# Kernel optimization log

Measured on AMD Instinct MI355X. Metric: run time of the kernel, lower is better.

## Reference

```python
import jax, jax.numpy as jnp
import numpy as np

NUM_HEADS = 16
HEAD_DIM = 64
MAX_REL = 128
NEG_INF = -1e30


def setup_inputs() -> dict:
    key = jax.random.key(0)
    ks = jax.random.split(key, 5)
    B, L, D = 2, 2048, 1024
    x = jax.random.normal(ks[0], (B, L, D), dtype=jnp.float32)
    key_padding_mask = jnp.zeros((B, L), dtype=bool)  # True = padded
    Wqkv = jax.random.normal(ks[1], (D, 3 * D), dtype=jnp.float32) * (D ** -0.5)
    bqkv = jnp.zeros((3 * D,), dtype=jnp.float32)
    Wout = jax.random.normal(ks[2], (D, D), dtype=jnp.float32) * (D ** -0.5)
    bout = jnp.zeros((D,), dtype=jnp.float32)
    bias_table = jax.random.normal(ks[3], (2 * MAX_REL + 1, NUM_HEADS), dtype=jnp.float32) * 0.02
    return {"x": x, "key_padding_mask": key_padding_mask, "Wqkv": Wqkv,
            "bqkv": bqkv, "Wout": Wout, "bout": bout, "bias_table": bias_table}


def _rel_bias(bias_table, L):
    # relative position index: clamp(k - q, -MAX_REL, MAX_REL) + MAX_REL -> [L, L]
    rel = jnp.arange(L)[None, :] - jnp.arange(L)[:, None]
    idx = jnp.clip(rel, -MAX_REL, MAX_REL) + MAX_REL
    return bias_table[idx].transpose(2, 0, 1)  # [H, L, L]


def reference(x, key_padding_mask, Wqkv, bqkv, Wout, bout, bias_table):
    B, L, D = x.shape
    H, hd = NUM_HEADS, HEAD_DIM
    qkv = x @ Wqkv + bqkv                      # [B, L, 3D]
    q, k, v = jnp.split(qkv, 3, axis=-1)
    q = q.reshape(B, L, H, hd).transpose(0, 2, 1, 3)  # [B, H, L, hd]
    k = k.reshape(B, L, H, hd).transpose(0, 2, 1, 3)
    v = v.reshape(B, L, H, hd).transpose(0, 2, 1, 3)
    scores = jnp.einsum('bhqd,bhkd->bhqk', q, k) * (hd ** -0.5)
    scores = scores + _rel_bias(bias_table, L)[None]   # [B, H, L, L]
    scores = jnp.where(key_padding_mask[:, None, None, :], NEG_INF, scores)
    attn = jax.nn.softmax(scores, axis=-1)
    out = jnp.einsum('bhqk,bhkd->bhqd', attn, v)       # [B, H, L, hd]
    out = out.transpose(0, 2, 1, 3).reshape(B, L, D)
    return out @ Wout + bout
```

## Files before the change

### kernel.cpp

```cpp
#include <hip/hip_runtime.h>
#include <hip/hip_bf16.h>
#include <stdint.h>

#define LSEQ 2048
#define BATCH 2
#define DMODEL 1024
#define NH 16
#define HD 64

typedef __attribute__((ext_vector_type(8))) short bf16x8;
typedef __attribute__((ext_vector_type(4))) float f32x4;

__device__ __forceinline__ short f2bf(float f) {
  union { float f; uint32_t u; } v; v.f = f;
  uint32_t r = v.u + 0x8000u;
  return (short)(r >> 16);
}

__device__ __forceinline__ uint32_t pack_bf16(float lo, float hi) {
  union { float f; uint32_t u; } a, b; a.f = lo; b.f = hi;
  uint32_t al = (a.u + 0x8000u) >> 16;
  uint32_t bh = (b.u + 0x8000u) & 0xFFFF0000u;
  return al | bh;
}

__device__ __forceinline__ float exp2_fast(float x) {
#if __has_builtin(__builtin_amdgcn_exp2f)
  return __builtin_amdgcn_exp2f(x);
#else
  float r; asm("v_exp_f32 %0, %1" : "=v"(r) : "v"(x)); return r;
#endif
}

__device__ __forceinline__ void gll16(const void* g, void* l) {
  __builtin_amdgcn_global_load_lds(
      (const __attribute__((address_space(1))) void*)g,
      (__attribute__((address_space(3))) void*)l, 16, 0, 0);
}

__global__ void cvt_bf16(const float* __restrict__ in, short* __restrict__ out, int n) {
  int i = (blockIdx.x * blockDim.x + threadIdx.x) * 4;
  if (i < n) {
    float4 v = *(const float4*)(in + i);
    short4 o;
    o.x = f2bf(v.x); o.y = f2bf(v.y); o.z = f2bf(v.z); o.w = f2bf(v.w);
    *(short4*)(out + i) = o;
  }
}

__global__ void transpose_cvt(const float* __restrict__ in, short* __restrict__ out,
                              int K, int N) {
  __shared__ float tile[32][33];
  int kb = blockIdx.x * 32, nb = blockIdx.y * 32;
  int tx = threadIdx.x & 31, ty = threadIdx.x >> 5;
  #pragma unroll
  for (int i = ty; i < 32; i += 8)
    tile[i][tx] = in[(size_t)(kb + i) * N + nb + tx];
  __syncthreads();
  #pragma unroll
  for (int i = ty; i < 32; i += 8)
    out[(size_t)(nb + i) * K + kb + tx] = f2bf(tile[tx][i]);
}

template <int EPI>
__global__ __launch_bounds__(256, 2) void gemm_bt(
    const short* __restrict__ A, const short* __restrict__ Bt,
    const float* __restrict__ bias, float* __restrict__ outf,
    short* __restrict__ q_out, short* __restrict__ k_out, short* __restrict__ v_out) {
  constexpr int K = 1024, BK = 32;
  __shared__ short Als[128 * BK];
  __shared__ short Bls[128 * BK];
  const int tid = threadIdx.x;
  const int lane = tid & 63;
  const int m0 = blockIdx.x * 128;
  const int n0 = blockIdx.y * 128;
  const int wid = tid >> 6;
  const int wm = (wid >> 1) * 64, wn = (wid & 1) * 64;

  f32x4 acc[4][4] = {};

  for (int kt = 0; kt < K / BK; ++kt) {
    const int k0 = kt * BK;
    __syncthreads();
    #pragma unroll
    for (int inst = 0; inst < 2; ++inst) {
      int c = inst * 256 + tid;
      int row = c >> 2, cc = (c & 3) * 8;
      gll16(A + (size_t)(m0 + row) * K + k0 + cc, Als + c * 8);
      gll16(Bt + (size_t)(n0 + row) * K + k0 + cc, Bls + c * 8);
    }
    __syncthreads();
    bf16x8 af[4], bfv[4];
    #pragma unroll
    for (int m = 0; m < 4; ++m)
      af[m] = *(const bf16x8*)(Als + (wm + m * 16 + (lane & 15)) * BK + (lane >> 4) * 8);
    #pragma unroll
    for (int n = 0; n < 4; ++n)
      bfv[n] = *(const bf16x8*)(Bls + (wn + n * 16 + (lane & 15)) * BK + (lane >> 4) * 8);
    #pragma unroll
    for (int m = 0; m < 4; ++m)
      #pragma unroll
      for (int n = 0; n < 4; ++n)
        acc[m][n] = __builtin_amdgcn_mfma_f32_16x16x32_bf16(af[m], bfv[n], acc[m][n], 0, 0, 0);
  }

  #pragma unroll
  for (int m = 0; m < 4; ++m) {
    #pragma unroll
    for (int n = 0; n < 4; ++n) {
      #pragma unroll
      for (int r = 0; r < 4; ++r) {
        int row = m0 + wm + m * 16 + (lane >> 4) * 4 + r;
        int col = n0 + wn + n * 16 + (lane & 15);
        float val = acc[m][n][r] + bias[col];
        if (EPI == 1) {
          outf[(size_t)row * DMODEL + col] = val;
        } else {
          int b = row >> 11, l = row & 2047;
          int which = col >> 10, rem = col & 1023;
          int hn = rem >> 6, d = rem & 63;
          size_t bh = (size_t)b * NH + hn;
          if (which == 0)       q_out[(bh * LSEQ + l) * HD + d] = f2bf(val * 0.1803368801f);
          else if (which == 1)  k_out[(bh * LSEQ + l) * HD + d] = f2bf(val);
          else                  v_out[(bh * HD + d) * LSEQ + l] = f2bf(val);
        }
      }
    }
  }
}

__global__ __launch_bounds__(256, 3) void attn_kernel(
    const short* __restrict__ qb, const short* __restrict__ kb,
    const short* __restrict__ vtb, const unsigned char* __restrict__ kpm,
    const float* __restrict__ bias_table, short* __restrict__ ob) {
  constexpr int NT = LSEQ / 64;
  __shared__ short Kls[2][64 * 64];
  __shared__ short Vls[2][64 * 64];
  __shared__ short Pls[4][16 * 64];
  __shared__ float biasc[257];
  __shared__ float maskls[LSEQ];
  __shared__ int flags[NT];

  const int tid = threadIdx.x, lane = tid & 63, wid = tid >> 6;
  const int g = lane >> 4, c = lane & 15;
  const int q0 = blockIdx.x * 64, h = blockIdx.y, b = blockIdx.z;
  const size_t bh = (size_t)b * NH + h;
  const short* qbase = qb + bh * LSEQ * HD;
  const short* kbase = kb + bh * LSEQ * HD;
  const short* vbase = vtb + bh * HD * LSEQ;

  const int qrow_frag = q0 + wid * 16 + c;
  bf16x8 qf[2];
  #pragma unroll
  for (int ks = 0; ks < 2; ++ks)
    qf[ks] = *(const bf16x8*)(qbase + (size_t)qrow_frag * HD + ks * 32 + g * 8);

  if (tid < NT) flags[tid] = 0;
  __syncthreads();
  for (int i = tid; i < 257; i += 256) biasc[i] = bias_table[i * NH + h] * 1.44269504f;
  for (int i = tid; i < LSEQ; i += 256) {
    unsigned char m = kpm[(size_t)b * LSEQ + i];
    maskls[i] = m ? -1e30f : 0.f;
    if (m) flags[i >> 6] = 1;
  }
  __syncthreads();
  const float cb_lo = biasc[0], cb_hi = biasc[256];
  int myflag = (lane < 32) ? flags[lane] : 0;
  const unsigned mbits = (unsigned)__ballot(myflag != 0);

  auto stage = [&](int t, int bbuf) {
    const int kv0s = t * 64;
    #pragma unroll
    for (int inst = 0; inst < 2; ++inst) {
      int cc0 = inst * 256 + tid;
      int row = cc0 >> 3, cc = cc0 & 7;
      int scc = cc ^ (row & 7);
      gll16(kbase + (size_t)(kv0s + row) * HD + scc * 8, &Kls[bbuf][cc0 * 8]);
      gll16(vbase + (size_t)row * LSEQ + kv0s + scc * 8, &Vls[bbuf][cc0 * 8]);
    }
  };

  f32x4 o[4], l_acc;
  #pragma unroll
  for (int nt = 0; nt < 4; ++nt) o[nt] = (f32x4){0.f, 0.f, 0.f, 0.f};
  l_acc = (f32x4){0.f, 0.f, 0.f, 0.f};

  bf16x8 onesf;
  #pragma unroll
  for (int j = 0; j < 8; ++j) onesf[j] = (short)0x3F80;

  char* pw = (char*)&Pls[wid][0];
  const int c7s = (c & 7) << 4;

  stage(0, 0);

  for (int t = 0; t < NT; ++t) {
    const int bb = t & 1;
    const int kv0 = t * 64;
    if (t < NT - 1) {
      stage(t + 1, bb ^ 1);
      asm volatile("s_waitcnt vmcnt(4) lgkmcnt(0)" ::: "memory");
    } else {
      asm volatile("s_waitcnt vmcnt(0) lgkmcnt(0)" ::: "memory");
    }
    __builtin_amdgcn_s_barrier();
    __builtin_amdgcn_sched_barrier(0);

    f32x4 st[4];
    #pragma unroll
    for (int nt = 0; nt < 4; ++nt) {
      f32x4 a = {};
      #pragma unroll
      for (int ks = 0; ks < 2; ++ks) {
        int krow = nt * 16 + c;
        int kbyte = (ks * 32 + g * 8) * 2;
        const bf16x8 kf =
            *(const bf16x8*)((const char*)&Kls[bb][0] + krow * 128 + (kbyte ^ ((krow & 7) << 4)));
        a = __builtin_amdgcn_mfma_f32_16x16x32_bf16(kf, qf[ks], a, 0, 0, 0);
      }
      st[nt] = a;
    }

    const int dqk = kv0 - q0;
    if (dqk >= 192 || dqk <= -192) {
      const float cb = dqk > 0 ? cb_hi : cb_lo;
      #pragma unroll
      for (int nt = 0; nt < 4; ++nt)
        #pragma unroll
        for (int r = 0; r < 4; ++r) st[nt][r] += cb;
    } else {
      const int q = q0 + wid * 16 + c;
      #pragma unroll
      for (int nt = 0; nt < 4; ++nt)
        #pragma unroll
        for (int r = 0; r < 4; ++r) {
          int rel = kv0 + nt * 16 + g * 4 + r - q;
          rel = rel < -128 ? -128 : (rel > 128 ? 128 : rel);
          st[nt][r] += biasc[rel + 128];
        }
    }
    if (mbits & (1u << t)) {
      #pragma unroll
      for (int nt = 0; nt < 4; ++nt)
        #pragma unroll
        for (int r = 0; r < 4; ++r)
          st[nt][r] += maskls[kv0 + nt * 16 + g * 4 + r];
    }

    #pragma unroll
    for (int nt = 0; nt < 4; ++nt) {
      uint32_t p01 = pack_bf16(exp2_fast(st[nt][0]), exp2_fast(st[nt][1]));
      uint32_t p23 = pack_bf16(exp2_fast(st[nt][2]), exp2_fast(st[nt][3]));
      uint2 w; w.x = p01; w.y = p23;
      *(uint2*)(pw + c * 128 + ((nt * 32 + g * 8) ^ c7s)) = w;
    }

    asm volatile("s_waitcnt lgkmcnt(0)" ::: "memory");
    __builtin_amdgcn_sched_barrier(0);

    #pragma unroll
    for (int ks = 0; ks < 2; ++ks) {
      const bf16x8 pa = *(const bf16x8*)(pw + c * 128 + ((ks * 64 + g * 16) ^ c7s));
      l_acc = __builtin_amdgcn_mfma_f32_16x16x32_bf16(pa, onesf, l_acc, 0, 0, 0);
      int pbyte = (ks * 32 + g * 8) * 2;
      #pragma unroll
      for (int nt = 0; nt < 4; ++nt) {
        int vrow = nt * 16 + c;
        const bf16x8 vf =
            *(const bf16x8*)((const char*)&Vls[bb][0] + vrow * 128 + (pbyte ^ ((vrow & 7) << 4)));
        o[nt] = __builtin_amdgcn_mfma_f32_16x16x32_bf16(pa, vf, o[nt], 0, 0, 0);
      }
    }

    __builtin_amdgcn_sched_barrier(0);
    __builtin_amdgcn_s_barrier();
  }

  #pragma unroll
  for (int r = 0; r < 4; ++r) {
    float inv = 1.f / l_acc[r];
    int qrow = q0 + wid * 16 + g * 4 + r;
    size_t obase = ((size_t)b * LSEQ + qrow) * DMODEL + (size_t)h * HD;
    #pragma unroll
    for (int nt = 0; nt < 4; ++nt)
      ob[obase + nt * 16 + c] = f2bf(o[nt][r] * inv);
  }
}

extern "C" void kernel_launch(void* const* d_in, const int* in_sizes, int n_in,
                              void* d_out, int out_size, void* d_ws, size_t ws_size,
                              hipStream_t stream) {
  (void)in_sizes; (void)n_in; (void)out_size; (void)ws_size;
  const float* x = (const float*)d_in[0];
  const unsigned char* kpm = (const unsigned char*)d_in[1];
  const float* Wqkv = (const float*)d_in[2];
  const float* bqkv = (const float*)d_in[3];
  const float* Wout = (const float*)d_in[4];
  const float* bout = (const float*)d_in[5];
  const float* btab = (const float*)d_in[6];
  float* out = (float*)d_out;

  short* ws = (short*)d_ws;
  short* xbf   = ws;
  short* wqkvT = xbf + 4194304;
  short* woutT = wqkvT + 3145728;
  short* qbuf  = woutT + 1048576;
  short* kbuf  = qbuf + 4194304;
  short* vtbuf = kbuf + 4194304;
  short* obuf  = vtbuf + 4194304;

  cvt_bf16<<<dim3(4096), dim3(256), 0, stream>>>(x, xbf, 4194304);
  transpose_cvt<<<dim3(32, 96), dim3(256), 0, stream>>>(Wqkv, wqkvT, 1024, 3072);
  transpose_cvt<<<dim3(32, 32), dim3(256), 0, stream>>>(Wout, woutT, 1024, 1024);

  gemm_bt<0><<<dim3(32, 24), dim3(256), 0, stream>>>(xbf, wqkvT, bqkv, nullptr,
                                                     qbuf, kbuf, vtbuf);
  attn_kernel<<<dim3(32, 16, 2), dim3(256), 0, stream>>>(qbuf, kbuf, vtbuf, kpm, btab, obuf);
  gemm_bt<1><<<dim3(32, 8), dim3(256), 0, stream>>>(obuf, woutT, bout, out,
                                                    nullptr, nullptr, nullptr);
}
```

Measured before the change: 156.5 us.

## Process 32 query rows per wave to reuse K/V tiles across two query groups

The attention kernel doubles its query tile from 64 to 128 rows per block. Each wave now handles two 16-row query groups, and every K and V fragment read from LDS feeds two MFMAs, halving K/V global and LDS traffic per query. The mask preprocessing is also simplified: a per-tile bitmask is built from vectorized byte loads, and the mask is read straight from global memory only on masked tiles, instead of a float mask array kept in LDS. In exchange the grid is half the size, register pressure is higher, and launch bounds drop to 2 blocks per CU, which lowers occupancy.

Result: faster. 137.6 us (-12.1%).

```diff
diff --git a/kernel.cpp b/kernel.cpp
--- a/kernel.cpp
+++ b/kernel.cpp
@@ -129,44 +129,47 @@
   }
 }
 
-__global__ __launch_bounds__(256, 3) void attn_kernel(
+__global__ __launch_bounds__(256, 2) void attn_kernel(
     const short* __restrict__ qb, const short* __restrict__ kb,
     const short* __restrict__ vtb, const unsigned char* __restrict__ kpm,
     const float* __restrict__ bias_table, short* __restrict__ ob) {
   constexpr int NT = LSEQ / 64;
   __shared__ short Kls[2][64 * 64];
   __shared__ short Vls[2][64 * 64];
-  __shared__ short Pls[4][16 * 64];
+  __shared__ short Pls[4][32 * 64];
   __shared__ float biasc[257];
-  __shared__ float maskls[LSEQ];
-  __shared__ int flags[NT];
+  __shared__ unsigned mbits_s;
 
   const int tid = threadIdx.x, lane = tid & 63, wid = tid >> 6;
   const int g = lane >> 4, c = lane & 15;
-  const int q0 = blockIdx.x * 64, h = blockIdx.y, b = blockIdx.z;
+  const int q0 = blockIdx.x * 128, h = blockIdx.y, b = blockIdx.z;
   const size_t bh = (size_t)b * NH + h;
   const short* qbase = qb + bh * LSEQ * HD;
   const short* kbase = kb + bh * LSEQ * HD;
   const short* vbase = vtb + bh * HD * LSEQ;
-
-  const int qrow_frag = q0 + wid * 16 + c;
-  bf16x8 qf[2];
-  #pragma unroll
-  for (int ks = 0; ks < 2; ++ks)
-    qf[ks] = *(const bf16x8*)(qbase + (size_t)qrow_frag * HD + ks * 32 + g * 8);
-
-  if (tid < NT) flags[tid] = 0;
+  const unsigned char* kpmb = kpm + (size_t)b * LSEQ;
+
+  bf16x8 qf[2][2];
+  #pragma unroll
+  for (int qg = 0; qg < 2; ++qg)
+    #pragma unroll
+    for (int ks = 0; ks < 2; ++ks) {
+      int qrow = q0 + wid * 32 + qg * 16 + c;
+      qf[qg][ks] = *(const bf16x8*)(qbase + (size_t)qrow * HD + ks * 32 + g * 8);
+    }
+
+  if (tid < 32) {
+    const uint4* mp = (const uint4*)(kpmb + tid * 64);
+    uint4 m0 = mp[0], m1 = mp[1], m2 = mp[2], m3 = mp[3];
+    unsigned anyb = m0.x | m0.y | m0.z | m0.w | m1.x | m1.y | m1.z | m1.w |
+                    m2.x | m2.y | m2.z | m2.w | m3.x | m3.y | m3.z | m3.w;
+    unsigned long long bal = __ballot(anyb != 0);
+    if (tid == 0) mbits_s = (unsigned)bal;
+  }
+  for (int i = tid; i < 257; i += 256) biasc[i] = bias_table[i * NH + h] * 1.44269504f;
   __syncthreads();
-  for (int i = tid; i < 257; i += 256) biasc[i] = bias_table[i * NH + h] * 1.44269504f;
-  for (int i = tid; i < LSEQ; i += 256) {
-    unsigned char m = kpm[(size_t)b * LSEQ + i];
-    maskls[i] = m ? -1e30f : 0.f;
-    if (m) flags[i >> 6] = 1;
-  }
-  __syncthreads();
+  const unsigned mbits = mbits_s;
   const float cb_lo = biasc[0], cb_hi = biasc[256];
-  int myflag = (lane < 32) ? flags[lane] : 0;
-  const unsigned mbits = (unsigned)__ballot(myflag != 0);
 
   auto stage = [&](int t, int bbuf) {
     const int kv0s = t * 64;
@@ -180,10 +183,13 @@
     }
   };
 
-  f32x4 o[4], l_acc;
-  #pragma unroll
-  for (int nt = 0; nt < 4; ++nt) o[nt] = (f32x4){0.f, 0.f, 0.f, 0.f};
-  l_acc = (f32x4){0.f, 0.f, 0.f, 0.f};
+  f32x4 o[4][2], l_acc[2];
+  #pragma unroll
+  for (int nt = 0; nt < 4; ++nt)
+    #pragma unroll
+    for (int qg = 0; qg < 2; ++qg) o[nt][qg] = (f32x4){0.f, 0.f, 0.f, 0.f};
+  l_acc[0] = (f32x4){0.f, 0.f, 0.f, 0.f};
+  l_acc[1] = (f32x4){0.f, 0.f, 0.f, 0.f};
 
   bf16x8 onesf;
   #pragma unroll
@@ -206,69 +212,83 @@
     __builtin_amdgcn_s_barrier();
     __builtin_amdgcn_sched_barrier(0);
 
-    f32x4 st[4];
+    f32x4 st[4][2];
     #pragma unroll
     for (int nt = 0; nt < 4; ++nt) {
-      f32x4 a = {};
+      f32x4 a0 = {}, a1 = {};
       #pragma unroll
       for (int ks = 0; ks < 2; ++ks) {
         int krow = nt * 16 + c;
-        int kbyte = (ks * 32 + g * 8) * 2;
+        int kbyte = ks * 64 + g * 16;
         const bf16x8 kf =
-            *(const bf16x8*)((const char*)&Kls[bb][0] + krow * 128 + (kbyte ^ ((krow & 7) << 4)));
-        a = __builtin_amdgcn_mfma_f32_16x16x32_bf16(kf, qf[ks], a, 0, 0, 0);
+            *(const bf16x8*)((const char*)&Kls[bb][0] + krow * 128 + (kbyte ^ c7s));
+        a0 = __builtin_amdgcn_mfma_f32_16x16x32_bf16(kf, qf[0][ks], a0, 0, 0, 0);
+        a1 = __builtin_amdgcn_mfma_f32_16x16x32_bf16(kf, qf[1][ks], a1, 0, 0, 0);
       }
-      st[nt] = a;
-    }
-
-    const int dqk = kv0 - q0;
-    if (dqk >= 192 || dqk <= -192) {
-      const float cb = dqk > 0 ? cb_hi : cb_lo;
+      st[nt][0] = a0; st[nt][1] = a1;
+    }
+
+    const int dw = kv0 - q0 - wid * 32;
+    if (dw >= 160 || dw <= -192) {
+      const float cb = dw > 0 ? cb_hi : cb_lo;
       #pragma unroll
       for (int nt = 0; nt < 4; ++nt)
         #pragma unroll
-        for (int r = 0; r < 4; ++r) st[nt][r] += cb;
+        for (int qg = 0; qg < 2; ++qg)
+          #pragma unroll
+          for (int r = 0; r < 4; ++r) st[nt][qg][r] += cb;
     } else {
-      const int q = q0 + wid * 16 + c;
+      #pragma unroll
+      for (int nt = 0; nt < 4; ++nt)
+        #pragma unroll
+        for (int qg = 0; qg < 2; ++qg) {
+          const int base = dw + nt * 16 + g * 4 - qg * 16 - c;
+          #pragma unroll
+          for (int r = 0; r < 4; ++r) {
+            int rel = base + r;
+            rel = rel < -128 ? -128 : (rel > 128 ? 128 : rel);
+            st[nt][qg][r] += biasc[rel + 128];
+          }
+        }
+    }
+    if (mbits & (1u << t)) {
       #pragma unroll
       for (int nt = 0; nt < 4; ++nt)
         #pragma unroll
         for (int r = 0; r < 4; ++r) {
-          int rel = kv0 + nt * 16 + g * 4 + r - q;
-          rel = rel < -128 ? -128 : (rel > 128 ? 128 : rel);
-          st[nt][r] += biasc[rel + 128];
+          float mk = kpmb[kv0 + nt * 16 + g * 4 + r] ? -1e30f : 0.f;
+          st[nt][0][r] += mk;
+          st[nt][1][r] += mk;
         }
     }
-    if (mbits & (1u << t)) {
-      #pragma unroll
-      for (int nt = 0; nt < 4; ++nt)
-        #pragma unroll
-        for (int r = 0; r < 4; ++r)
-          st[nt][r] += maskls[kv0 + nt * 16 + g * 4 + r];
-    }
-
-    #pragma unroll
-    for (int nt = 0; nt < 4; ++nt) {
-      uint32_t p01 = pack_bf16(exp2_fast(st[nt][0]), exp2_fast(st[nt][1]));
-      uint32_t p23 = pack_bf16(exp2_fast(st[nt][2]), exp2_fast(st[nt][3]));
-      uint2 w; w.x = p01; w.y = p23;
-      *(uint2*)(pw + c * 128 + ((nt * 32 + g * 8) ^ c7s)) = w;
-    }
+
+    #pragma unroll
+    for (int qg = 0; qg < 2; ++qg)
+      #pragma unroll
+      for (int nt = 0; nt < 4; ++nt) {
+        uint32_t p01 = pack_bf16(exp2_fast(st[nt][qg][0]), exp2_fast(st[nt][qg][1]));
+        uint32_t p23 = pack_bf16(exp2_fast(st[nt][qg][2]), exp2_fast(st[nt][qg][3]));
+        uint2 w; w.x = p01; w.y = p23;
+        *(uint2*)(pw + (qg * 16 + c) * 128 + ((nt * 32 + g * 8) ^ c7s)) = w;
+      }
 
     asm volatile("s_waitcnt lgkmcnt(0)" ::: "memory");
     __builtin_amdgcn_sched_barrier(0);
 
     #pragma unroll
     for (int ks = 0; ks < 2; ++ks) {
-      const bf16x8 pa = *(const bf16x8*)(pw + c * 128 + ((ks * 64 + g * 16) ^ c7s));
-      l_acc = __builtin_amdgcn_mfma_f32_16x16x32_bf16(pa, onesf, l_acc, 0, 0, 0);
-      int pbyte = (ks * 32 + g * 8) * 2;
+      const int pbyte = ks * 64 + g * 16;
+      bf16x8 pa0 = *(const bf16x8*)(pw + c * 128 + (pbyte ^ c7s));
+      bf16x8 pa1 = *(const bf16x8*)(pw + (16 + c) * 128 + (pbyte ^ c7s));
+      l_acc[0] = __builtin_amdgcn_mfma_f32_16x16x32_bf16(pa0, onesf, l_acc[0], 0, 0, 0);
+      l_acc[1] = __builtin_amdgcn_mfma_f32_16x16x32_bf16(pa1, onesf, l_acc[1], 0, 0, 0);
       #pragma unroll
       for (int nt = 0; nt < 4; ++nt) {
         int vrow = nt * 16 + c;
         const bf16x8 vf =
-            *(const bf16x8*)((const char*)&Vls[bb][0] + vrow * 128 + (pbyte ^ ((vrow & 7) << 4)));
-        o[nt] = __builtin_amdgcn_mfma_f32_16x16x32_bf16(pa, vf, o[nt], 0, 0, 0);
+            *(const bf16x8*)((const char*)&Vls[bb][0] + vrow * 128 + (pbyte ^ c7s));
+        o[nt][0] = __builtin_amdgcn_mfma_f32_16x16x32_bf16(pa0, vf, o[nt][0], 0, 0, 0);
+        o[nt][1] = __builtin_amdgcn_mfma_f32_16x16x32_bf16(pa1, vf, o[nt][1], 0, 0, 0);
       }
     }
 
@@ -277,14 +297,16 @@
   }
 
   #pragma unroll
-  for (int r = 0; r < 4; ++r) {
-    float inv = 1.f / l_acc[r];
-    int qrow = q0 + wid * 16 + g * 4 + r;
-    size_t obase = ((size_t)b * LSEQ + qrow) * DMODEL + (size_t)h * HD;
-    #pragma unroll
-    for (int nt = 0; nt < 4; ++nt)
-      ob[obase + nt * 16 + c] = f2bf(o[nt][r] * inv);
-  }
+  for (int qg = 0; qg < 2; ++qg)
+    #pragma unroll
+    for (int r = 0; r < 4; ++r) {
+      float inv = 1.f / l_acc[qg][r];
+      int qrow = q0 + wid * 32 + qg * 16 + g * 4 + r;
+      size_t obase = ((size_t)b * LSEQ + qrow) * DMODEL + (size_t)h * HD;
+      #pragma unroll
+      for (int nt = 0; nt < 4; ++nt)
+        ob[obase + nt * 16 + c] = f2bf(o[nt][qg][r] * inv);
+    }
 }
 
 extern "C" void kernel_launch(void* const* d_in, const int* in_sizes, int n_in,
@@ -315,7 +337,7 @@
 
   gemm_bt<0><<<dim3(32, 24), dim3(256), 0, stream>>>(xbf, wqkvT, bqkv, nullptr,
                                                      qbuf, kbuf, vtbuf);
-  attn_kernel<<<dim3(32, 16, 2), dim3(256), 0, stream>>>(qbuf, kbuf, vtbuf, kpm, btab, obuf);
+  attn_kernel<<<dim3(16, 16, 2), dim3(256), 0, stream>>>(qbuf, kbuf, vtbuf, kpm, btab, obuf);
   gemm_bt<1><<<dim3(32, 8), dim3(256), 0, stream>>>(obuf, woutT, bout, out,
                                                     nullptr, nullptr, nullptr);
 }
```
